# Kernel tuning notes

Measured on AMD Instinct MI355X. Metric: run time of the kernel, lower is better.

Reference implementation:

```python
import jax, jax.numpy as jnp
import numpy as np

T, B, D, H = 256, 128, 128, 1024
MEL = 48           # preprocess.melodyRange
MELODY_COEFF = 0.5
FORGET_BIAS = 1.0  # TF BasicLSTMCell default


def setup_inputs() -> dict:
    key = jax.random.key(0)
    ks = jax.random.split(key, 8)
    s = 0.05
    return {
        "inSeq": jax.random.normal(ks[0], (T, B, D), dtype=jnp.float32),
        "targetSeq": jax.random.randint(ks[1], (T, B, 2), 0, MEL).astype(jnp.int64),
        "W1": jax.random.normal(ks[2], (D + H, 4 * H), dtype=jnp.float32) * s,
        "b1": jnp.zeros((4 * H,), dtype=jnp.float32),
        "W2": jax.random.normal(ks[3], (2 * H, 4 * H), dtype=jnp.float32) * s,
        "b2": jnp.zeros((4 * H,), dtype=jnp.float32),
        "outW": jax.random.normal(ks[4], (H, D), dtype=jnp.float32) * s,
        "outB": jnp.zeros((D,), dtype=jnp.float32),
    }


def _lstm_cell(x, c, h, W, b):
    # TF BasicLSTMCell: gates in (i, j, f, o) order, forget_bias added to f
    z = jnp.concatenate([x, h], axis=-1) @ W + b
    i, j, f, o = jnp.split(z, 4, axis=-1)
    c_new = c * jax.nn.sigmoid(f + FORGET_BIAS) + jax.nn.sigmoid(i) * jnp.tanh(j)
    h_new = jnp.tanh(c_new) * jax.nn.sigmoid(o)
    return c_new, h_new


def _forward(inSeq, targetSeq, W1, b1, W2, b2, outW, outB):
    dt = inSeq.dtype
    zero = jnp.zeros((B, H), dtype=dt)

    def step(carry, x):
        c1, h1, c2, h2 = carry
        c1, h1 = _lstm_cell(x, c1, h1, W1, b1)
        c2, h2 = _lstm_cell(h1, c2, h2, W2, b2)
        return (c1, h1, c2, h2), h2

    _, outputs = jax.lax.scan(step, (zero, zero, zero, zero), inSeq)  # [T,B,H]
    logits = outputs @ outW + outB                                    # [T,B,D]

    mel_logits = logits[..., :MEL]
    har_logits = logits[..., MEL:]

    # probs: per-timestep dual softmax, concatenated
    probs = jnp.concatenate(
        [jax.nn.softmax(mel_logits, axis=-1), jax.nn.softmax(har_logits, axis=-1)],
        axis=-1,
    )

    # dual sparse softmax cross-entropy
    mel_lp = jax.nn.log_softmax(mel_logits, axis=-1)
    har_lp = jax.nn.log_softmax(har_logits, axis=-1)
    mel_ce = -jnp.take_along_axis(mel_lp, targetSeq[..., 0:1], axis=-1)[..., 0]
    har_ce = -jnp.take_along_axis(har_lp, targetSeq[..., 1:2], axis=-1)[..., 0]
    losses = MELODY_COEFF * mel_ce + (1.0 - MELODY_COEFF) * har_ce
    loss = jnp.sum(losses) / T / B
    return probs, loss


def reference(inSeq, targetSeq, W1, b1, W2, b2, outW, outB):
    return _forward(inSeq, targetSeq, W1, b1, W2, b2, outW, outB)
```

## Files before the change

kernel.cpp:

```cpp
#include <hip/hip_runtime.h>
#include <cstdint>
#include <cstddef>

#define T_ 256
#define B_ 128
#define D_ 128
#define H_ 1024
#define K1_ 1152
#define K2_ 2048

#define R_ 32

typedef __bf16 bf16x8 __attribute__((ext_vector_type(8)));
typedef short s8 __attribute__((ext_vector_type(8)));
typedef float f32x4 __attribute__((ext_vector_type(4)));

__device__ __forceinline__ unsigned short f2bf(float f) {
  unsigned int u = __builtin_bit_cast(unsigned int, f);
  u += 0x7fff + ((u >> 16) & 1);
  return (unsigned short)(u >> 16);
}
__device__ __forceinline__ float sigm(float x) { return 1.f / (1.f + __expf(-x)); }
__device__ __forceinline__ float tanh_(float x) { return 1.f - 2.f / (__expf(2.f * x) + 1.f); }

__device__ __forceinline__ f32x4 mfma16(s8 a, s8 b, f32x4 c) {
  return __builtin_amdgcn_mfma_f32_16x16x32_bf16(
      __builtin_bit_cast(bf16x8, a), __builtin_bit_cast(bf16x8, b), c, 0, 0, 0);
}

__device__ __forceinline__ void st_bypass_short(unsigned short* p, unsigned int v) {
  asm volatile("global_store_short %0, %1, off sc0 sc1" :: "v"(p), "v"(v) : "memory");
}
__device__ __forceinline__ void st_flag(int* p, int v) {
  asm volatile("global_store_dword %0, %1, off sc0 sc1" :: "v"(p), "v"(v) : "memory");
}

__device__ __forceinline__ void wave_wait1(const int* p, int want) {
  for (;;) {
    int4 v;
    asm volatile("global_load_dwordx4 %0, %1, off sc0 sc1\n\ts_waitcnt vmcnt(0)"
                 : "=v"(v) : "v"(p) : "memory");
    int ok = (v.x >= want) && (v.y >= want) && (v.z >= want) && (v.w >= want);
    if (__all(ok)) break;
    __builtin_amdgcn_s_sleep(3);
  }
}
__device__ __forceinline__ void wave_wait2(const int* pa, int wa,
                                           const int* pb, int wb) {
  for (;;) {
    int4 a, b;
    asm volatile("global_load_dwordx4 %0, %2, off sc0 sc1\n\t"
                 "global_load_dwordx4 %1, %3, off sc0 sc1\n\t"
                 "s_waitcnt vmcnt(0)"
                 : "=v"(a), "=v"(b) : "v"(pa), "v"(pb) : "memory");
    int ok = (a.x >= wa) && (a.y >= wa) && (a.z >= wa) && (a.w >= wa) &&
             (b.x >= wb) && (b.y >= wb) && (b.z >= wb) && (b.w >= wb);
    if (__all(ok)) break;
    __builtin_amdgcn_s_sleep(3);
  }
}

__global__ void prep_misc(const float* __restrict__ inSeq,
                          const float* __restrict__ outW,
                          unsigned short* __restrict__ xbf,
                          unsigned short* __restrict__ outWp,
                          unsigned short* __restrict__ h1b,
                          unsigned short* __restrict__ h1r,
                          unsigned short* __restrict__ h2all,
                          float* __restrict__ c1, float* __restrict__ c2,
                          float* __restrict__ loss,
                          int* __restrict__ f1, int* __restrict__ f2)
{
  int i = blockIdx.x * 256 + threadIdx.x;
  if (i < T_ * B_ * D_) xbf[i] = f2bf(inSeq[i]);
  if (i < B_ * H_) {
    c1[i] = 0.f; c2[i] = 0.f;
    h1b[B_ * H_ + i] = 0;
    if (h1r) h1r[(size_t)(R_ - 1) * B_ * H_ + i] = 0;
    h2all[i] = 0;
  }
  if (i < H_ * D_) {
    int c = i >> 10, k = i & 1023;
    outWp[i] = f2bf(outW[(size_t)k * D_ + c]);
  }
  if (f1 && i < 256) { f1[i] = 0; f2[i] = 0; }
  if (i == 0) loss[0] = 0.f;
}

__global__ void pack_w(const float* __restrict__ src, unsigned short* __restrict__ dst, int K)
{
  __shared__ float tile[64][65];
  int k0 = blockIdx.x * 64, j0 = blockIdx.y * 64, g = blockIdx.z;
  int tid = threadIdx.x;
#pragma unroll
  for (int e = 0; e < 16; ++e) {
    int li = e * 256 + tid;
    int kl = li >> 6, jl = li & 63;
    tile[kl][jl] = src[(size_t)(k0 + kl) * 4096 + g * 1024 + j0 + jl];
  }
  __syncthreads();
#pragma unroll
  for (int e = 0; e < 16; ++e) {
    int li = e * 256 + tid;
    int jl = li >> 6, kl = li & 63;
    dst[(size_t)((j0 + jl) * 4 + g) * K + k0 + kl] = f2bf(tile[kl][jl]);
  }
}

__global__ __launch_bounds__(256, 2) void phase_kernel(
    int p,
    const unsigned short* __restrict__ xbf,
    const unsigned short* __restrict__ W1p,
    const unsigned short* __restrict__ W2p,
    const float* __restrict__ b1,
    const float* __restrict__ b2,
    unsigned short* __restrict__ h1b,
    unsigned short* __restrict__ h2all,
    float* __restrict__ c1,
    float* __restrict__ c2)
{
  __shared__ float red[4][2048];
  const int bid = blockIdx.x;
  const bool isL2 = bid >= 256;
  if (!isL2 && p >= T_) return;
  if (isL2 && p == 0) return;
  const int jb = isL2 ? (bid - 256) : bid;
  const int mt = jb & 1, nt = jb >> 1;
  const int t = isL2 ? (p - 1) : p;
  const int r0 = mt * 64, c0 = nt * 32;
  const int tid = threadIdx.x;
  const int wid = tid >> 6, lane = tid & 63;
  const int quad = lane >> 4, l15 = lane & 15;
  const int kseg = quad * 8;

  const unsigned short* hsrc = h1b + (size_t)((p + 1) & 1) * (B_ * H_);

  f32x4 acc[4][2];
#pragma unroll
  for (int i = 0; i < 4; ++i)
#pragma unroll
    for (int j = 0; j < 2; ++j) acc[i][j] = (f32x4){0.f, 0.f, 0.f, 0.f};

  int arow[4], bcol[2];
#pragma unroll
  for (int i = 0; i < 4; ++i) arow[i] = r0 + i * 16 + l15;
#pragma unroll
  for (int j = 0; j < 2; ++j) bcol[j] = c0 + j * 16 + l15;

  if (!isL2) {
    const unsigned short* xt = xbf + (size_t)t * (B_ * D_);
    const int cpw = 9;
    const int kcbase = wid * cpw;
    s8 a[4], b[2], an[4], bn[2];
    auto LD = [&](int kc, s8* A, s8* Bv) {
      int kk = kc * 32 + kseg;
      if (kk < D_) {
#pragma unroll
        for (int i = 0; i < 4; ++i) A[i] = *(const s8*)(xt + (size_t)arow[i] * D_ + kk);
      } else {
#pragma unroll
        for (int i = 0; i < 4; ++i) A[i] = *(const s8*)(hsrc + (size_t)arow[i] * H_ + (kk - D_));
      }
#pragma unroll
      for (int j = 0; j < 2; ++j) Bv[j] = *(const s8*)(W1p + (size_t)bcol[j] * K1_ + kk);
    };
    LD(kcbase, a, b);
    for (int c = 0; c < cpw; ++c) {
      if (c + 1 < cpw) LD(kcbase + c + 1, an, bn);
#pragma unroll
      for (int i = 0; i < 4; ++i)
#pragma unroll
        for (int j = 0; j < 2; ++j) acc[i][j] = mfma16(a[i], b[j], acc[i][j]);
#pragma unroll
      for (int i = 0; i < 4; ++i) a[i] = an[i];
      b[0] = bn[0]; b[1] = bn[1];
    }
  } else {
    const unsigned short* h2prev = h2all + (size_t)t * (B_ * H_);
    const int cpw = 16;
    const int kcbase = wid * cpw;
    s8 a[4], b[2], an[4], bn[2];
    auto LD = [&](int kc, s8* A, s8* Bv) {
      int kk = kc * 32 + kseg;
      if (kk < H_) {
#pragma unroll
        for (int i = 0; i < 4; ++i) A[i] = *(const s8*)(hsrc + (size_t)arow[i] * H_ + kk);
      } else {
#pragma unroll
        for (int i = 0; i < 4; ++i) A[i] = *(const s8*)(h2prev + (size_t)arow[i] * H_ + (kk - H_));
      }
#pragma unroll
      for (int j = 0; j < 2; ++j) Bv[j] = *(const s8*)(W2p + (size_t)bcol[j] * K2_ + kk);
    };
    LD(kcbase, a, b);
    for (int c = 0; c < cpw; ++c) {
      if (c + 1 < cpw) LD(kcbase + c + 1, an, bn);
#pragma unroll
      for (int i = 0; i < 4; ++i)
#pragma unroll
        for (int j = 0; j < 2; ++j) acc[i][j] = mfma16(a[i], b[j], acc[i][j]);
#pragma unroll
      for (int i = 0; i < 4; ++i) a[i] = an[i];
      b[0] = bn[0]; b[1] = bn[1];
    }
  }

#pragma unroll
  for (int i = 0; i < 4; ++i)
#pragma unroll
    for (int j = 0; j < 2; ++j)
#pragma unroll
      for (int r = 0; r < 4; ++r)
        red[wid][(i * 16 + quad * 4 + r) * 32 + (j * 16 + l15)] = acc[i][j][r];
  __syncthreads();
#pragma unroll
  for (int it = 0; it < 8; ++it) {
    int e = it * 256 + tid;
    red[0][e] = red[0][e] + red[1][e] + red[2][e] + red[3][e];
  }
  __syncthreads();

  const float* bias = isL2 ? b2 : b1;
  float* cst = isL2 ? c2 : c1;
  unsigned short* hout = isL2 ? (h2all + (size_t)(t + 1) * (B_ * H_))
                              : (h1b + (size_t)(p & 1) * (B_ * H_));
#pragma unroll
  for (int it = 0; it < 2; ++it) {
    int s = it * 256 + tid;
    int row = s >> 3, u = s & 7;
    int jg = (c0 >> 2) + u;
    float zi = red[0][row * 32 + u * 4 + 0] + bias[0 * H_ + jg];
    float zj = red[0][row * 32 + u * 4 + 1] + bias[1 * H_ + jg];
    float zf = red[0][row * 32 + u * 4 + 2] + bias[2 * H_ + jg];
    float zo = red[0][row * 32 + u * 4 + 3] + bias[3 * H_ + jg];
    int rg = r0 + row;
    float co = cst[(size_t)rg * H_ + jg];
    float cn = co * sigm(zf + 1.0f) + sigm(zi) * tanh_(zj);
    float hn = tanh_(cn) * sigm(zo);
    cst[(size_t)rg * H_ + jg] = cn;
    hout[(size_t)rg * H_ + jg] = f2bf(hn);
  }
}

__global__ __attribute__((amdgpu_waves_per_eu(2, 2))) __launch_bounds__(256)
void lstm_persistent(
    const unsigned short* __restrict__ xbf,
    const unsigned short* __restrict__ W1p,
    const unsigned short* __restrict__ W2p,
    const float* __restrict__ b1,
    const float* __restrict__ b2,
    unsigned short* __restrict__ h1r,
    unsigned short* __restrict__ h2all,
    int* __restrict__ f1,
    int* __restrict__ f2)
{
  __shared__ float red[4][2048];
  const int bid = blockIdx.x;
  const bool isL2 = bid >= 256;
  const int jb = isL2 ? (bid - 256) : bid;
  const int mt = jb & 1, nt = jb >> 1;
  const int r0 = mt * 64, c0 = nt * 32;
  const int tid = threadIdx.x;
  const int wid = tid >> 6, lane = tid & 63;
  const int quad = lane >> 4, l15 = lane & 15;
  const int kseg = quad * 8;
  const int lane4 = lane * 4;

  int arow[4], bcol[2];
#pragma unroll
  for (int i = 0; i < 4; ++i) arow[i] = r0 + i * 16 + l15;
#pragma unroll
  for (int j = 0; j < 2; ++j) bcol[j] = c0 + j * 16 + l15;

  const float* bias = isL2 ? b2 : b1;
  int ridx[2];
  unsigned hoff[2];
  float bz[2][4], creg[2];
#pragma unroll
  for (int it = 0; it < 2; ++it) {
    int s = it * 256 + tid;
    int row = s >> 3, u = s & 7;
    int jg = (c0 >> 2) + u;
    ridx[it] = row * 32 + u * 4;
    hoff[it] = (unsigned)((r0 + row) * H_ + jg);
#pragma unroll
    for (int g = 0; g < 4; ++g) bz[it][g] = bias[g * H_ + jg];
    creg[it] = 0.f;
  }

  if (!isL2) {
    const int kcbase = wid * 9;
    s8 bw[9][2];
#pragma unroll
    for (int c = 0; c < 9; ++c) {
      int kk = (kcbase + c) * 32 + kseg;
      bw[c][0] = *(const s8*)(W1p + (size_t)bcol[0] * K1_ + kk);
      bw[c][1] = *(const s8*)(W1p + (size_t)bcol[1] * K1_ + kk);
    }
#pragma unroll
    for (int c = 0; c < 9; ++c)
      asm volatile("" : "+v"(bw[c][0]), "+v"(bw[c][1]));

    for (int t = 0; t < T_; ++t) {
      if (wid == 0) {
        if ((t & 15) == 0) wave_wait2(f1 + lane4, t, f2 + lane4, t - 16);
        else               wave_wait1(f1 + lane4, t);
      }
      __syncthreads();
      if ((t & (R_ - 1)) == 0 && t)
        __builtin_amdgcn_fence(__ATOMIC_ACQUIRE, "agent");

      const unsigned short* hsrc = h1r + (size_t)((t + R_ - 1) & (R_ - 1)) * (B_ * H_);
      const unsigned short* xt = xbf + (size_t)t * (B_ * D_);
      f32x4 acc[4][2];
#pragma unroll
      for (int i = 0; i < 4; ++i)
#pragma unroll
        for (int j = 0; j < 2; ++j) acc[i][j] = (f32x4){0.f, 0.f, 0.f, 0.f};
      s8 a[4], an[4];
      auto LD = [&](int kc, s8* A) {
        int kk = kc * 32 + kseg;
        if (kk < D_) {
#pragma unroll
          for (int i = 0; i < 4; ++i) A[i] = *(const s8*)(xt + (size_t)arow[i] * D_ + kk);
        } else {
#pragma unroll
          for (int i = 0; i < 4; ++i) A[i] = *(const s8*)(hsrc + (size_t)arow[i] * H_ + (kk - D_));
        }
      };
      LD(kcbase, a);
#pragma unroll
      for (int c = 0; c < 9; ++c) {
        if (c + 1 < 9) LD(kcbase + c + 1, an);
#pragma unroll
        for (int i = 0; i < 4; ++i)
#pragma unroll
          for (int j = 0; j < 2; ++j) acc[i][j] = mfma16(a[i], bw[c][j], acc[i][j]);
#pragma unroll
        for (int i = 0; i < 4; ++i) a[i] = an[i];
      }
#pragma unroll
      for (int i = 0; i < 4; ++i)
#pragma unroll
        for (int j = 0; j < 2; ++j)
#pragma unroll
          for (int r = 0; r < 4; ++r)
            red[wid][(i * 16 + quad * 4 + r) * 32 + (j * 16 + l15)] = acc[i][j][r];
      __syncthreads();
#pragma unroll
      for (int it = 0; it < 8; ++it) {
        int e = it * 256 + tid;
        red[0][e] = red[0][e] + red[1][e] + red[2][e] + red[3][e];
      }
      __syncthreads();
      unsigned short* hout = h1r + (size_t)(t & (R_ - 1)) * (B_ * H_);
#pragma unroll
      for (int it = 0; it < 2; ++it) {
        float zi = red[0][ridx[it] + 0] + bz[it][0];
        float zj = red[0][ridx[it] + 1] + bz[it][1];
        float zf = red[0][ridx[it] + 2] + bz[it][2];
        float zo = red[0][ridx[it] + 3] + bz[it][3];
        float cn = creg[it] * sigm(zf + 1.0f) + sigm(zi) * tanh_(zj);
        float hn = tanh_(cn) * sigm(zo);
        creg[it] = cn;
        st_bypass_short(hout + hoff[it], (unsigned int)f2bf(hn));
      }
      asm volatile("s_waitcnt vmcnt(0)" ::: "memory");
      __syncthreads();
      if (tid == 0) st_flag(f1 + jb, t + 1);
    }
  } else {
    const int kcbase = wid * 16;
    s8 bw[16][2];
#pragma unroll
    for (int c = 0; c < 16; ++c) {
      int kk = (kcbase + c) * 32 + kseg;
      bw[c][0] = *(const s8*)(W2p + (size_t)bcol[0] * K2_ + kk);
      bw[c][1] = *(const s8*)(W2p + (size_t)bcol[1] * K2_ + kk);
    }
#pragma unroll
    for (int c = 0; c < 16; ++c)
      asm volatile("" : "+v"(bw[c][0]), "+v"(bw[c][1]));

    for (int t = 0; t < T_; ++t) {
      if (wid == 0) wave_wait2(f1 + lane4, t + 1, f2 + lane4, t);
      __syncthreads();
      if ((t & (R_ - 1)) == 0 && t)
        __builtin_amdgcn_fence(__ATOMIC_ACQUIRE, "agent");

      const unsigned short* hsrc = h1r + (size_t)(t & (R_ - 1)) * (B_ * H_);
      const unsigned short* h2prev = h2all + (size_t)t * (B_ * H_);
      f32x4 acc[4][2];
#pragma unroll
      for (int i = 0; i < 4; ++i)
#pragma unroll
        for (int j = 0; j < 2; ++j) acc[i][j] = (f32x4){0.f, 0.f, 0.f, 0.f};
      s8 a[4], an[4];
      auto LD = [&](int kc, s8* A) {
        int kk = kc * 32 + kseg;
        if (kk < H_) {
#pragma unroll
          for (int i = 0; i < 4; ++i) A[i] = *(const s8*)(hsrc + (size_t)arow[i] * H_ + kk);
        } else {
#pragma unroll
          for (int i = 0; i < 4; ++i) A[i] = *(const s8*)(h2prev + (size_t)arow[i] * H_ + (kk - H_));
        }
      };
      LD(kcbase, a);
#pragma unroll
      for (int c = 0; c < 16; ++c) {
        if (c + 1 < 16) LD(kcbase + c + 1, an);
#pragma unroll
        for (int i = 0; i < 4; ++i)
#pragma unroll
          for (int j = 0; j < 2; ++j) acc[i][j] = mfma16(a[i], bw[c][j], acc[i][j]);
#pragma unroll
        for (int i = 0; i < 4; ++i) a[i] = an[i];
      }
#pragma unroll
      for (int i = 0; i < 4; ++i)
#pragma unroll
        for (int j = 0; j < 2; ++j)
#pragma unroll
          for (int r = 0; r < 4; ++r)
            red[wid][(i * 16 + quad * 4 + r) * 32 + (j * 16 + l15)] = acc[i][j][r];
      __syncthreads();
#pragma unroll
      for (int it = 0; it < 8; ++it) {
        int e = it * 256 + tid;
        red[0][e] = red[0][e] + red[1][e] + red[2][e] + red[3][e];
      }
      __syncthreads();
      unsigned short* hout = h2all + (size_t)(t + 1) * (B_ * H_);
#pragma unroll
      for (int it = 0; it < 2; ++it) {
        float zi = red[0][ridx[it] + 0] + bz[it][0];
        float zj = red[0][ridx[it] + 1] + bz[it][1];
        float zf = red[0][ridx[it] + 2] + bz[it][2];
        float zo = red[0][ridx[it] + 3] + bz[it][3];
        float cn = creg[it] * sigm(zf + 1.0f) + sigm(zi) * tanh_(zj);
        float hn = tanh_(cn) * sigm(zo);
        creg[it] = cn;
        st_bypass_short(hout + hoff[it], (unsigned int)f2bf(hn));
      }
      asm volatile("s_waitcnt vmcnt(0)" ::: "memory");
      __syncthreads();
      if (tid == 0) st_flag(f2 + jb, t + 1);
    }
  }
}

__global__ __launch_bounds__(256, 1) void proj_kernel(
    const unsigned short* __restrict__ h2flat,
    const unsigned short* __restrict__ outWp,
    const float* __restrict__ outB,
    const int* __restrict__ targets,
    float* __restrict__ out,
    float* __restrict__ loss)
{
  __shared__ float lg[128][129];
  __shared__ float red2[256];
  const int r0 = blockIdx.x * 128;
  const int tid = threadIdx.x;
  const int wid = tid >> 6, lane = tid & 63;
  const int quad = lane >> 4, l15 = lane & 15;
  const int wr = (wid & 1) * 64, wc = (wid >> 1) * 64;
  const int kseg = quad * 8;

  f32x4 acc[4][4];
#pragma unroll
  for (int i = 0; i < 4; ++i)
#pragma unroll
    for (int j = 0; j < 4; ++j) acc[i][j] = (f32x4){0.f, 0.f, 0.f, 0.f};

  int arow[4], bcolv[4];
#pragma unroll
  for (int i = 0; i < 4; ++i) arow[i] = r0 + wr + i * 16 + l15;
#pragma unroll
  for (int j = 0; j < 4; ++j) bcolv[j] = wc + j * 16 + l15;

  s8 a[4], b[4], an[4], bn[4];
  auto LD = [&](int kc, s8* A, s8* Bv) {
    int kk = kc * 32 + kseg;
#pragma unroll
    for (int i = 0; i < 4; ++i) A[i] = *(const s8*)(h2flat + (size_t)arow[i] * H_ + kk);
#pragma unroll
    for (int j = 0; j < 4; ++j) Bv[j] = *(const s8*)(outWp + (size_t)bcolv[j] * H_ + kk);
  };
  LD(0, a, b);
  for (int c = 0; c < 32; ++c) {
    if (c + 1 < 32) LD(c + 1, an, bn);
#pragma unroll
    for (int i = 0; i < 4; ++i)
#pragma unroll
      for (int j = 0; j < 4; ++j) acc[i][j] = mfma16(a[i], b[j], acc[i][j]);
#pragma unroll
    for (int i = 0; i < 4; ++i) a[i] = an[i];
#pragma unroll
    for (int j = 0; j < 4; ++j) b[j] = bn[j];
  }

#pragma unroll
  for (int i = 0; i < 4; ++i)
#pragma unroll
    for (int j = 0; j < 4; ++j)
#pragma unroll
      for (int r = 0; r < 4; ++r)
        lg[wr + i * 16 + quad * 4 + r][wc + j * 16 + l15] = acc[i][j][r] + outB[bcolv[j]];
  __syncthreads();

  const int row = tid >> 1, half = tid & 1;
  const int cbeg = half ? 48 : 0, cend = half ? 128 : 48;
  float m = -1e30f;
  for (int c = cbeg; c < cend; ++c) m = fmaxf(m, lg[row][c]);
  float s = 0.f;
  for (int c = cbeg; c < cend; ++c) s += __expf(lg[row][c] - m);
  float rinv = 1.f / s;
  float* orow = out + (size_t)(r0 + row) * D_;
  for (int c = cbeg; c < cend; ++c) orow[c] = __expf(lg[row][c] - m) * rinv;

  int tg = targets[(size_t)(r0 + row) * 2 + half];
  int tc = half ? (48 + tg) : tg;
  float ce = -(lg[row][tc] - m - logf(s));
  red2[tid] = 0.5f * ce;
  __syncthreads();
  for (int o = 128; o > 0; o >>= 1) {
    if (tid < o) red2[tid] += red2[tid + o];
    __syncthreads();
  }
  if (tid == 0) atomicAdd(loss, red2[0]);
}

__global__ void finalize_loss(const float* __restrict__ loss, float* __restrict__ out)
{
  out[(size_t)T_ * B_ * D_] = loss[0] * (1.f / (float)(T_ * B_));
}

extern "C" void kernel_launch(void* const* d_in, const int* in_sizes, int n_in,
                              void* d_out, int out_size, void* d_ws, size_t ws_size,
                              hipStream_t stream)
{
  const float* inSeq = (const float*)d_in[0];
  const int* targets = (const int*)d_in[1];
  const float* W1 = (const float*)d_in[2];
  const float* b1 = (const float*)d_in[3];
  const float* W2 = (const float*)d_in[4];
  const float* b2 = (const float*)d_in[5];
  const float* outW = (const float*)d_in[6];
  const float* outB = (const float*)d_in[7];
  float* out = (float*)d_out;

  char* w = (char*)d_ws;
  auto alloc = [&](size_t bytes) {
    char* r = w;
    w += (bytes + 255) & ~(size_t)255;
    return r;
  };
  unsigned short* W1p = (unsigned short*)alloc((size_t)4096 * K1_ * 2);
  unsigned short* W2p = (unsigned short*)alloc((size_t)4096 * K2_ * 2);
  unsigned short* xbf = (unsigned short*)alloc((size_t)T_ * B_ * D_ * 2);
  unsigned short* h1b = (unsigned short*)alloc((size_t)2 * B_ * H_ * 2);
  unsigned short* h2all = (unsigned short*)alloc((size_t)(T_ + 1) * B_ * H_ * 2);
  float* c1 = (float*)alloc((size_t)B_ * H_ * 4);
  float* c2 = (float*)alloc((size_t)B_ * H_ * 4);
  unsigned short* outWp = (unsigned short*)alloc((size_t)H_ * D_ * 2);
  float* loss = (float*)alloc(256);
  int* f1 = (int*)alloc(256 * 4);
  int* f2 = (int*)alloc(256 * 4);
  unsigned short* h1r = (unsigned short*)alloc((size_t)R_ * B_ * H_ * 2);

  const bool fits = ((size_t)(w - (char*)d_ws) <= ws_size);
  if (!fits) { f1 = nullptr; f2 = nullptr; h1r = nullptr; }

  prep_misc<<<dim3((T_ * B_ * D_) / 256), dim3(256), 0, stream>>>(
      inSeq, outW, xbf, outWp, h1b, h1r, h2all, c1, c2, loss, f1, f2);
  pack_w<<<dim3(K1_ / 64, 16, 4), dim3(256), 0, stream>>>(W1, W1p, K1_);
  pack_w<<<dim3(K2_ / 64, 16, 4), dim3(256), 0, stream>>>(W2, W2p, K2_);

  hipError_t ce = hipErrorUnknown;
  if (fits) {
    void* kargs[] = {(void*)&xbf, (void*)&W1p, (void*)&W2p, (void*)&b1,
                     (void*)&b2,  (void*)&h1r, (void*)&h2all,
                     (void*)&f1,  (void*)&f2};
    ce = hipLaunchCooperativeKernel((const void*)lstm_persistent,
                                    dim3(512), dim3(256), kargs, 0, stream);
  }
  if (ce != hipSuccess) {
    (void)hipGetLastError();
    for (int p = 0; p <= T_; ++p)
      phase_kernel<<<dim3(512), dim3(256), 0, stream>>>(
          p, xbf, W1p, W2p, b1, b2, h1b, h2all, c1, c2);
  }

  proj_kernel<<<dim3(256), dim3(256), 0, stream>>>(
      h2all + (size_t)B_ * H_, outWp, outB, targets, out, loss);
  finalize_loss<<<dim3(1), dim3(1), 0, stream>>>(loss, out);
}
```

Before: 5.098 ms.

## Double persistent LSTM block to 8 waves and stream weights from global

Changes the persistent LSTM kernel from 256 to 512 threads per block, splitting the K reduction across 8 waves instead of 4, with an 8-way LDS reduction and one gate element per thread. Weight fragments are no longer pinned in registers for the whole run. They are reloaded from global memory (the packed W1p/W2p) every timestep alongside the activations. The aim is more wave-level parallelism and shorter per-wave MFMA chains on the serial critical path. The cost is re-fetching roughly 2×(K1+K2)×H bf16 weights each step through L2, plus a larger LDS footprint that may hurt residency of the cooperative launch.

```diff
diff --git a/kernel.cpp b/kernel.cpp
--- a/kernel.cpp
+++ b/kernel.cpp
@@ -242,8 +242,7 @@
   }
 }
 
-__global__ __attribute__((amdgpu_waves_per_eu(2, 2))) __launch_bounds__(256)
-void lstm_persistent(
+__global__ __launch_bounds__(512, 4) void lstm_persistent(
     const unsigned short* __restrict__ xbf,
     const unsigned short* __restrict__ W1p,
     const unsigned short* __restrict__ W2p,
@@ -254,7 +253,7 @@
     int* __restrict__ f1,
     int* __restrict__ f2)
 {
-  __shared__ float red[4][2048];
+  __shared__ float red[8][2048];
   const int bid = blockIdx.x;
   const bool isL2 = bid >= 256;
   const int jb = isL2 ? (bid - 256) : bid;
@@ -273,33 +272,17 @@
   for (int j = 0; j < 2; ++j) bcol[j] = c0 + j * 16 + l15;
 
   const float* bias = isL2 ? b2 : b1;
-  int ridx[2];
-  unsigned hoff[2];
-  float bz[2][4], creg[2];
-#pragma unroll
-  for (int it = 0; it < 2; ++it) {
-    int s = it * 256 + tid;
-    int row = s >> 3, u = s & 7;
-    int jg = (c0 >> 2) + u;
-    ridx[it] = row * 32 + u * 4;
-    hoff[it] = (unsigned)((r0 + row) * H_ + jg);
-#pragma unroll
-    for (int g = 0; g < 4; ++g) bz[it][g] = bias[g * H_ + jg];
-    creg[it] = 0.f;
-  }
+  const int erow = tid >> 3, eu = tid & 7;
+  const int jg = nt * 8 + eu;
+  const int ridx = erow * 32 + eu * 4;
+  const unsigned hoff = (unsigned)((r0 + erow) * H_ + jg);
+  float bz[4], creg = 0.f;
+#pragma unroll
+  for (int g = 0; g < 4; ++g) bz[g] = bias[g * H_ + jg];
 
   if (!isL2) {
-    const int kcbase = wid * 9;
-    s8 bw[9][2];
-#pragma unroll
-    for (int c = 0; c < 9; ++c) {
-      int kk = (kcbase + c) * 32 + kseg;
-      bw[c][0] = *(const s8*)(W1p + (size_t)bcol[0] * K1_ + kk);
-      bw[c][1] = *(const s8*)(W1p + (size_t)bcol[1] * K1_ + kk);
-    }
-#pragma unroll
-    for (int c = 0; c < 9; ++c)
-      asm volatile("" : "+v"(bw[c][0]), "+v"(bw[c][1]));
+    const int cpw = (wid < 4) ? 5 : 4;
+    const int kcbase = (wid < 4) ? (wid * 5) : (20 + (wid - 4) * 4);
 
     for (int t = 0; t < T_; ++t) {
       if (wid == 0) {
@@ -317,8 +300,8 @@
       for (int i = 0; i < 4; ++i)
 #pragma unroll
         for (int j = 0; j < 2; ++j) acc[i][j] = (f32x4){0.f, 0.f, 0.f, 0.f};
-      s8 a[4], an[4];
-      auto LD = [&](int kc, s8* A) {
+      s8 a[4], b[2], an[4], bn[2];
+      auto LD = [&](int kc, s8* A, s8* Bv) {
         int kk = kc * 32 + kseg;
         if (kk < D_) {
 #pragma unroll
@@ -327,17 +310,19 @@
 #pragma unroll
           for (int i = 0; i < 4; ++i) A[i] = *(const s8*)(hsrc + (size_t)arow[i] * H_ + (kk - D_));
         }
+#pragma unroll
+        for (int j = 0; j < 2; ++j) Bv[j] = *(const s8*)(W1p + (size_t)bcol[j] * K1_ + kk);
       };
-      LD(kcbase, a);
-#pragma unroll
-      for (int c = 0; c < 9; ++c) {
-        if (c + 1 < 9) LD(kcbase + c + 1, an);
+      LD(kcbase, a, b);
+      for (int c = 0; c < cpw; ++c) {
+        if (c + 1 < cpw) LD(kcbase + c + 1, an, bn);
 #pragma unroll
         for (int i = 0; i < 4; ++i)
 #pragma unroll
-          for (int j = 0; j < 2; ++j) acc[i][j] = mfma16(a[i], bw[c][j], acc[i][j]);
+          for (int j = 0; j < 2; ++j) acc[i][j] = mfma16(a[i], b[j], acc[i][j]);
 #pragma unroll
         for (int i = 0; i < 4; ++i) a[i] = an[i];
+        b[0] = bn[0]; b[1] = bn[1];
       }
 #pragma unroll
       for (int i = 0; i < 4; ++i)
@@ -348,39 +333,30 @@
             red[wid][(i * 16 + quad * 4 + r) * 32 + (j * 16 + l15)] = acc[i][j][r];
       __syncthreads();
 #pragma unroll
-      for (int it = 0; it < 8; ++it) {
-        int e = it * 256 + tid;
-        red[0][e] = red[0][e] + red[1][e] + red[2][e] + red[3][e];
+      for (int it = 0; it < 4; ++it) {
+        int e = it * 512 + tid;
+        red[0][e] = ((red[0][e] + red[1][e]) + (red[2][e] + red[3][e])) +
+                    ((red[4][e] + red[5][e]) + (red[6][e] + red[7][e]));
       }
       __syncthreads();
       unsigned short* hout = h1r + (size_t)(t & (R_ - 1)) * (B_ * H_);
-#pragma unroll
-      for (int it = 0; it < 2; ++it) {
-        float zi = red[0][ridx[it] + 0] + bz[it][0];
-        float zj = red[0][ridx[it] + 1] + bz[it][1];
-        float zf = red[0][ridx[it] + 2] + bz[it][2];
-        float zo = red[0][ridx[it] + 3] + bz[it][3];
-        float cn = creg[it] * sigm(zf + 1.0f) + sigm(zi) * tanh_(zj);
+      {
+        float zi = red[0][ridx + 0] + bz[0];
+        float zj = red[0][ridx + 1] + bz[1];
+        float zf = red[0][ridx + 2] + bz[2];
+        float zo = red[0][ridx + 3] + bz[3];
+        float cn = creg * sigm(zf + 1.0f) + sigm(zi) * tanh_(zj);
         float hn = tanh_(cn) * sigm(zo);
-        creg[it] = cn;
-        st_bypass_short(hout + hoff[it], (unsigned int)f2bf(hn));
+        creg = cn;
+        st_bypass_short(hout + hoff, (unsigned int)f2bf(hn));
       }
       asm volatile("s_waitcnt vmcnt(0)" ::: "memory");
       __syncthreads();
       if (tid == 0) st_flag(f1 + jb, t + 1);
     }
   } else {
-    const int kcbase = wid * 16;
-    s8 bw[16][2];
-#pragma unroll
-    for (int c = 0; c < 16; ++c) {
-      int kk = (kcbase + c) * 32 + kseg;
-      bw[c][0] = *(const s8*)(W2p + (size_t)bcol[0] * K2_ + kk);
-      bw[c][1] = *(const s8*)(W2p + (size_t)bcol[1] * K2_ + kk);
-    }
-#pragma unroll
-    for (int c = 0; c < 16; ++c)
-      asm volatile("" : "+v"(bw[c][0]), "+v"(bw[c][1]));
+    const int cpw = 8;
+    const int kcbase = wid * 8;
 
     for (int t = 0; t < T_; ++t) {
       if (wid == 0) wave_wait2(f1 + lane4, t + 1, f2 + lane4, t);
@@ -395,8 +371,8 @@
       for (int i = 0; i < 4; ++i)
 #pragma unroll
         for (int j = 0; j < 2; ++j) acc[i][j] = (f32x4){0.f, 0.f, 0.f, 0.f};
-      s8 a[4], an[4];
-      auto LD = [&](int kc, s8* A) {
+      s8 a[4], b[2], an[4], bn[2];
+      auto LD = [&](int kc, s8* A, s8* Bv) {
         int kk = kc * 32 + kseg;
         if (kk < H_) {
 #pragma unroll
@@ -405,17 +381,19 @@
 #pragma unroll
           for (int i = 0; i < 4; ++i) A[i] = *(const s8*)(h2prev + (size_t)arow[i] * H_ + (kk - H_));
         }
+#pragma unroll
+        for (int j = 0; j < 2; ++j) Bv[j] = *(const s8*)(W2p + (size_t)bcol[j] * K2_ + kk);
       };
-      LD(kcbase, a);
-#pragma unroll
-      for (int c = 0; c < 16; ++c) {
-        if (c + 1 < 16) LD(kcbase + c + 1, an);
+      LD(kcbase, a, b);
+      for (int c = 0; c < cpw; ++c) {
+        if (c + 1 < cpw) LD(kcbase + c + 1, an, bn);
 #pragma unroll
         for (int i = 0; i < 4; ++i)
 #pragma unroll
-          for (int j = 0; j < 2; ++j) acc[i][j] = mfma16(a[i], bw[c][j], acc[i][j]);
+          for (int j = 0; j < 2; ++j) acc[i][j] = mfma16(a[i], b[j], acc[i][j]);
 #pragma unroll
         for (int i = 0; i < 4; ++i) a[i] = an[i];
+        b[0] = bn[0]; b[1] = bn[1];
       }
 #pragma unroll
       for (int i = 0; i < 4; ++i)
@@ -426,22 +404,22 @@
             red[wid][(i * 16 + quad * 4 + r) * 32 + (j * 16 + l15)] = acc[i][j][r];
       __syncthreads();
 #pragma unroll
-      for (int it = 0; it < 8; ++it) {
-        int e = it * 256 + tid;
-        red[0][e] = red[0][e] + red[1][e] + red[2][e] + red[3][e];
+      for (int it = 0; it < 4; ++it) {
+        int e = it * 512 + tid;
+        red[0][e] = ((red[0][e] + red[1][e]) + (red[2][e] + red[3][e])) +
+                    ((red[4][e] + red[5][e]) + (red[6][e] + red[7][e]));
       }
       __syncthreads();
       unsigned short* hout = h2all + (size_t)(t + 1) * (B_ * H_);
-#pragma unroll
-      for (int it = 0; it < 2; ++it) {
-        float zi = red[0][ridx[it] + 0] + bz[it][0];
-        float zj = red[0][ridx[it] + 1] + bz[it][1];
-        float zf = red[0][ridx[it] + 2] + bz[it][2];
-        float zo = red[0][ridx[it] + 3] + bz[it][3];
-        float cn = creg[it] * sigm(zf + 1.0f) + sigm(zi) * tanh_(zj);
+      {
+        float zi = red[0][ridx + 0] + bz[0];
+        float zj = red[0][ridx + 1] + bz[1];
+        float zf = red[0][ridx + 2] + bz[2];
+        float zo = red[0][ridx + 3] + bz[3];
+        float cn = creg * sigm(zf + 1.0f) + sigm(zi) * tanh_(zj);
         float hn = tanh_(cn) * sigm(zo);
-        creg[it] = cn;
-        st_bypass_short(hout + hoff[it], (unsigned int)f2bf(hn));
+        creg = cn;
+        st_bypass_short(hout + hoff, (unsigned int)f2bf(hn));
       }
       asm volatile("s_waitcnt vmcnt(0)" ::: "memory");
       __syncthreads();
@@ -583,7 +561,7 @@
                      (void*)&b2,  (void*)&h1r, (void*)&h2all,
                      (void*)&f1,  (void*)&f2};
     ce = hipLaunchCooperativeKernel((const void*)lstm_persistent,
-                                    dim3(512), dim3(256), kargs, 0, stream);
+                                    dim3(512), dim3(512), kargs, 0, stream);
   }
   if (ce != hipSuccess) {
     (void)hipGetLastError();
```

New measurement: 8.075 ms. 58.4% more time.
